# Optimization experiments

Hardware: AMD Instinct MI355X
Metric: run time of the kernel (lower is better)

## Reference

```python
import jax, jax.numpy as jnp
import numpy as np

ALPHA = 2.0
INF = 1e12  # sentinel 'infinity' for the distance transform (fp32-safe)


def _dt1d(f):
    """Exact 1D squared Euclidean distance transform along the last axis.
    d[i] = min_j ( f[j] + (i - j)^2 ).  Brute-force separable form.
    f: [..., N] -> [..., N]
    """
    n = f.shape[-1]
    i = jnp.arange(n, dtype=f.dtype)
    cost = (i[:, None] - i[None, :]) ** 2          # [N, N]
    return jnp.min(f[..., None, :] + cost, axis=-1)


def _edt(mask):
    """Euclidean distance of True pixels to the nearest False pixel
    (matches scipy.ndimage.distance_transform_edt on a binary mask).
    mask: bool [..., H, W] -> float [..., H, W]
    """
    f = jnp.where(mask, jnp.asarray(INF, jnp.float32), 0.0)
    f = _dt1d(f)                                     # pass along W
    f = _dt1d(jnp.swapaxes(f, -1, -2))               # pass along H
    f = jnp.swapaxes(f, -1, -2)
    return jnp.sqrt(jnp.minimum(f, INF))


def _distance_field(imgs):
    """imgs: [B, C, H, W] in [0,1]. Per (b,c): fg_dist/max + bg_dist/max."""
    fg_mask = imgs > 0.5
    bg_mask = ~fg_mask
    fg = _edt(fg_mask)
    bg = _edt(bg_mask)
    fg_any = jnp.any(fg_mask, axis=(-2, -1), keepdims=True)
    bg_any = jnp.any(bg_mask, axis=(-2, -1), keepdims=True)
    fg_n = fg / jnp.maximum(jnp.max(fg, axis=(-2, -1), keepdims=True), 1e-12)
    bg_n = bg / jnp.maximum(jnp.max(bg, axis=(-2, -1), keepdims=True), 1e-12)
    field = jnp.where(fg_any, fg_n + jnp.where(bg_any, bg_n, 0.0), 0.0)
    return field


def setup_inputs() -> dict:
    key = jax.random.key(0)
    k1, k2, k3 = jax.random.split(key, 3)
    B, C, H, W = 4, 2, 256, 256
    preds = jax.random.normal(k1, (B, C, H, W), dtype=jnp.float32)
    targets = jax.random.uniform(k2, (B, C, H, W), dtype=jnp.float32)
    labels = jax.random.randint(k3, (B,), 0, 2).astype(jnp.int64)
    return {"preds": preds, "targets": targets, "labels": labels}


def reference(preds, targets, labels):
    p = jax.nn.sigmoid(preds)
    # distance field is computed under no_grad in the original
    preds_dt = _distance_field(p)
    targets_dt = _distance_field(targets)
    distance = jax.lax.stop_gradient(preds_dt ** ALPHA + targets_dt ** ALPHA)
    preds_error = (p - targets) ** 2
    hd_loss = jnp.mean(preds_error * distance)
    return hd_loss
```

## Files before the change

kernel.cpp:

```cpp
#include <hip/hip_runtime.h>
#include <math.h>

#define HH 256
#define WW 256
#define NIMG 8
#define NF 32
#define FLDSZ (HH * WW)
#define NELEM (NIMG * FLDSZ)
#define LARGE (1 << 27)
#define BIGD (1 << 20)
#define BIGC (1 << 26)

#define BMP_OFF 0
#define BMT_OFF (64u * 1024)
#define APA_OFF (128u * 1024)
#define MPA_OFF (132u * 1024)

__global__ __launch_bounds__(256) void k_bitmap(
    const float* __restrict__ preds, const float* __restrict__ targets,
    unsigned long long* __restrict__ bmP, unsigned long long* __restrict__ bmT)
{
    const int img = blockIdx.x >> 5;
    const int rg  = blockIdx.x & 31;
    const int c   = threadIdx.x;
    const int lane = c & 63, wv = c >> 6;

    const size_t ibase = ((size_t)img * HH + rg * 8) * WW;
#pragma unroll
    for (int r8 = 0; r8 < 8; ++r8) {
        float pv = preds[ibase + r8 * WW + c];
        float tv = targets[ibase + r8 * WW + c];
        unsigned long long bp = __ballot(pv > 0.0f);
        unsigned long long bt = __ballot(tv > 0.5f);
        if (lane == 0) {
            const int row = rg * 8 + r8;
            bmP[((size_t)img * HH + row) * 4 + wv] = bp;
            bmT[((size_t)img * HH + row) * 4 + wv] = bt;
        }
    }
}

__device__ __forceinline__ int win_rowd2(const unsigned long long* __restrict__ sbm,
                                         int j, int wq, int sh)
{
    unsigned long long cur = sbm[j * 4 + wq];
    unsigned long long lw  = (wq > 0) ? sbm[j * 4 + wq - 1] : 0ull;
    unsigned long long rw  = (wq < 3) ? sbm[j * 4 + wq + 1] : 0ull;
    unsigned long long A = cur >> sh;
    if (sh) A |= rw << (64 - sh);
    int dR = A ? __builtin_ctzll(A) : 1000;
    unsigned long long L = (sh == 63) ? cur : (cur & ((1ull << (sh + 1)) - 1ull));
    int dL;
    if (L)       dL = sh - (63 - __builtin_clzll(L));
    else if (lw) dL = sh + 1 + __builtin_clzll(lw);
    else         dL = 1000;
    int d = min(dR, dL);
    return (d <= 255) ? d * d : BIGC;
}

__device__ __forceinline__ int full_rowd(const unsigned long long* __restrict__ sbm,
                                         int j, int c)
{
    int bestd = BIGD;
#pragma unroll
    for (int w = 0; w < 4; ++w) {
        unsigned long long mm = sbm[j * 4 + w];
        if (!mm) continue;
        const int base = w * 64;
        int d;
        if (base + 63 < c) {
            d = c - (base + 63 - __builtin_clzll(mm));
        } else if (base > c) {
            d = base + __builtin_ctzll(mm) - c;
        } else {
            const int t = c - base;
            unsigned long long lowm = (t == 63) ? mm : (mm & ((1ull << (t + 1)) - 1ull));
            unsigned long long him  = mm >> t;
            int dl = lowm ? (t - (63 - __builtin_clzll(lowm))) : BIGD;
            int dr = him  ? __builtin_ctzll(him) : BIGD;
            d = min(dl, dr);
        }
        bestd = min(bestd, d);
    }
    return bestd;
}

__global__ __launch_bounds__(256) void k_dtloss(
    const float* __restrict__ preds, const float* __restrict__ targets,
    const unsigned long long* __restrict__ bmP,
    const unsigned long long* __restrict__ bmT,
    double* __restrict__ Apart, int* __restrict__ Mpart)
{
    const int f   = blockIdx.x >> 4;
    const int rg  = blockIdx.x & 15;
    const int img = f >> 2;
    const int k   = f & 3;
    const int c   = threadIdx.x;
    const int wq  = c >> 6, sh = c & 63;

    __shared__ unsigned long long sbm[HH * 4];

    const unsigned long long* g = (k < 2) ? (bmP + (size_t)img * HH * 4)
                                          : (bmT + (size_t)img * HH * 4);
    const bool inv = ((k & 1) == 0);
#pragma unroll
    for (int q = 0; q < 4; ++q) {
        unsigned long long w = g[q * 256 + c];
        sbm[q * 256 + c] = inv ? ~w : w;
    }
    __syncthreads();

    const int i0 = rg * 16;
    int rw9[9];
#pragma unroll
    for (int q = 0; q < 9; ++q) {
        const int j = i0 - 4 + q;
        rw9[q] = ((unsigned)j < HH) ? win_rowd2(sbm, j, wq, sh) : BIGC;
    }

    double accA = 0.0;
    int mx = 0;

    for (int ii = 0; ii < 16; ++ii) {
        const int i = i0 + ii;

        int best = rw9[4];
        best = min(best, min(rw9[3], rw9[5]) + 1);
        best = min(best, min(rw9[2], rw9[6]) + 4);
        best = min(best, min(rw9[1], rw9[7]) + 9);
        best = min(best, min(rw9[0], rw9[8]) + 16);

        if (__any(best > 16)) {
            int d0 = full_rowd(sbm, i, c);
            int eb = (d0 <= 255) ? d0 * d0 : LARGE;
            for (int r = 1; r < HH; ++r) {
                if (__all(r * r >= eb)) break;
                const int jd = i - r, ju = i + r;
                if (jd >= 0) {
                    int d = full_rowd(sbm, jd, c);
                    if (d <= 255) eb = min(eb, d * d + r * r);
                }
                if (ju < HH) {
                    int d = full_rowd(sbm, ju, c);
                    if (d <= 255) eb = min(eb, d * d + r * r);
                }
            }
            best = eb;
        }

        const size_t idx = ((size_t)img * HH + i) * WW + c;
        float x = preds[idx];
        float t = targets[idx];
        float p = 1.0f / (1.0f + expf(-x));
        float err = (p - t) * (p - t);
        accA += (double)err * (double)best;
        mx = max(mx, best);

#pragma unroll
        for (int q = 0; q < 8; ++q) rw9[q] = rw9[q + 1];
        const int jn = i + 5;
        rw9[8] = ((unsigned)jn < HH) ? win_rowd2(sbm, jn, wq, sh) : BIGC;
    }

#pragma unroll
    for (int off = 32; off > 0; off >>= 1) {
        accA += __shfl_down(accA, off);
        mx = max(mx, __shfl_down(mx, off));
    }
    __shared__ double wA[4];
    __shared__ int    wM[4];
    const int lane = threadIdx.x & 63, wid = threadIdx.x >> 6;
    if (lane == 0) { wA[wid] = accA; wM[wid] = mx; }
    __syncthreads();
    if (threadIdx.x == 0) {
        double a = wA[0] + wA[1] + wA[2] + wA[3];
        int m = max(max(wM[0], wM[1]), max(wM[2], wM[3]));
        Apart[blockIdx.x] = a;
        Mpart[blockIdx.x] = m;
    }
}

__global__ __launch_bounds__(512) void k_final2(
    const double* __restrict__ Apart, const int* __restrict__ Mpart,
    float* __restrict__ out)
{
    const int t = threadIdx.x;
    double v = Apart[t];
    int m = Mpart[t];
#pragma unroll
    for (int off = 8; off > 0; off >>= 1) {
        v += __shfl_down(v, off);
        m = max(m, __shfl_down(m, off));
    }
    __shared__ double sA[NF];
    __shared__ int    sM[NF];
    if ((t & 15) == 0) { sA[t >> 4] = v; sM[t >> 4] = m; }
    __syncthreads();
    if (t == 0) {
        double loss = 0.0;
        for (int img = 0; img < NIMG; ++img) {
            const double a0 = sA[img * 4 + 0], a1 = sA[img * 4 + 1];
            const double a2 = sA[img * 4 + 2], a3 = sA[img * 4 + 3];
            const int m0 = sM[img * 4 + 0], m1 = sM[img * 4 + 1];
            const int m2 = sM[img * 4 + 2], m3 = sM[img * 4 + 3];
            if (m0 > 0) { loss += a0 / (double)m0; if (m1 > 0) loss += a1 / (double)m1; }
            if (m2 > 0) { loss += a2 / (double)m2; if (m3 > 0) loss += a3 / (double)m3; }
        }
        out[0] = (float)(loss / (double)NELEM);
    }
}

extern "C" void kernel_launch(void* const* d_in, const int* in_sizes, int n_in,
                              void* d_out, int out_size, void* d_ws, size_t ws_size,
                              hipStream_t stream)
{
    const float* preds   = (const float*)d_in[0];
    const float* targets = (const float*)d_in[1];
    float* out = (float*)d_out;

    char* ws = (char*)d_ws;
    unsigned long long* bmP = (unsigned long long*)(ws + BMP_OFF);
    unsigned long long* bmT = (unsigned long long*)(ws + BMT_OFF);
    double* Apart           = (double*)(ws + APA_OFF);
    int*    Mpart           = (int*)(ws + MPA_OFF);

    k_bitmap<<<NIMG * 32, 256, 0, stream>>>(preds, targets, bmP, bmT);
    k_dtloss<<<NF * 16,   256, 0, stream>>>(preds, targets, bmP, bmT, Apart, Mpart);
    k_final2<<<1,         512, 0, stream>>>(Apart, Mpart, out);
}
```

Before: 75.09 us.

## Compute all four distance fields per block with shared bitmaps and finer row split

```diff
diff --git a/kernel.cpp b/kernel.cpp
--- a/kernel.cpp
+++ b/kernel.cpp
@@ -14,11 +14,13 @@
 #define BMP_OFF 0
 #define BMT_OFF (64u * 1024)
 #define APA_OFF (128u * 1024)
-#define MPA_OFF (132u * 1024)
+#define MPA_OFF (144u * 1024)
+
+typedef unsigned long long u64;
 
 __global__ __launch_bounds__(256) void k_bitmap(
     const float* __restrict__ preds, const float* __restrict__ targets,
-    unsigned long long* __restrict__ bmP, unsigned long long* __restrict__ bmT)
+    u64* __restrict__ bmP, u64* __restrict__ bmT)
 {
     const int img = blockIdx.x >> 5;
     const int rg  = blockIdx.x & 31;
@@ -30,8 +32,8 @@
     for (int r8 = 0; r8 < 8; ++r8) {
         float pv = preds[ibase + r8 * WW + c];
         float tv = targets[ibase + r8 * WW + c];
-        unsigned long long bp = __ballot(pv > 0.0f);
-        unsigned long long bt = __ballot(tv > 0.5f);
+        u64 bp = __ballot(pv > 0.0f);
+        u64 bt = __ballot(tv > 0.5f);
         if (lane == 0) {
             const int row = rg * 8 + r8;
             bmP[((size_t)img * HH + row) * 4 + wv] = bp;
@@ -40,31 +42,38 @@
     }
 }
 
-__device__ __forceinline__ int win_rowd2(const unsigned long long* __restrict__ sbm,
-                                         int j, int wq, int sh)
-{
-    unsigned long long cur = sbm[j * 4 + wq];
-    unsigned long long lw  = (wq > 0) ? sbm[j * 4 + wq - 1] : 0ull;
-    unsigned long long rw  = (wq < 3) ? sbm[j * 4 + wq + 1] : 0ull;
-    unsigned long long A = cur >> sh;
-    if (sh) A |= rw << (64 - sh);
-    int dR = A ? __builtin_ctzll(A) : 1000;
-    unsigned long long L = (sh == 63) ? cur : (cur & ((1ull << (sh + 1)) - 1ull));
-    int dL;
-    if (L)       dL = sh - (63 - __builtin_clzll(L));
-    else if (lw) dL = sh + 1 + __builtin_clzll(lw);
-    else         dL = 1000;
-    int d = min(dR, dL);
-    return (d <= 255) ? d * d : BIGC;
-}
-
-__device__ __forceinline__ int full_rowd(const unsigned long long* __restrict__ sbm,
-                                         int j, int c)
+__device__ __forceinline__ void win_pair(const u64* __restrict__ sm, int j,
+                                         int wq, int sh, int out[2])
+{
+    const u64 cur = sm[j * 4 + wq];
+    const u64 lwr = (wq > 0) ? sm[j * 4 + wq - 1] : 0ull;
+    const u64 rwr = (wq < 3) ? sm[j * 4 + wq + 1] : 0ull;
+#pragma unroll
+    for (int pol = 0; pol < 2; ++pol) {
+        const u64 cc = pol ? ~cur : cur;
+        const u64 lw = pol ? ((wq > 0) ? ~lwr : 0ull) : lwr;
+        const u64 rw = pol ? ((wq < 3) ? ~rwr : 0ull) : rwr;
+        u64 A = cc >> sh;
+        if (sh) A |= rw << (64 - sh);
+        int dR = A ? __builtin_ctzll(A) : 1000;
+        u64 L = (sh == 63) ? cc : (cc & ((1ull << (sh + 1)) - 1ull));
+        int dL;
+        if (L)       dL = sh - (63 - __builtin_clzll(L));
+        else if (lw) dL = sh + 1 + __builtin_clzll(lw);
+        else         dL = 1000;
+        int d = min(dR, dL);
+        out[pol] = (d <= 255) ? d * d : BIGC;
+    }
+}
+
+__device__ __forceinline__ int full_rowd_f(const u64* __restrict__ sm, int j,
+                                           int c, bool inv)
 {
     int bestd = BIGD;
 #pragma unroll
     for (int w = 0; w < 4; ++w) {
-        unsigned long long mm = sbm[j * 4 + w];
+        u64 mm = sm[j * 4 + w];
+        if (inv) mm = ~mm;
         if (!mm) continue;
         const int base = w * 64;
         int d;
@@ -74,8 +83,8 @@
             d = base + __builtin_ctzll(mm) - c;
         } else {
             const int t = c - base;
-            unsigned long long lowm = (t == 63) ? mm : (mm & ((1ull << (t + 1)) - 1ull));
-            unsigned long long him  = mm >> t;
+            u64 lowm = (t == 63) ? mm : (mm & ((1ull << (t + 1)) - 1ull));
+            u64 him  = mm >> t;
             int dl = lowm ? (t - (63 - __builtin_clzll(lowm))) : BIGD;
             int dr = him  ? __builtin_ctzll(him) : BIGD;
             d = min(dl, dr);
@@ -85,126 +94,174 @@
     return bestd;
 }
 
+__device__ __forceinline__ int exact_scan(const u64* __restrict__ sm, int i,
+                                          int c, bool inv)
+{
+    int d0 = full_rowd_f(sm, i, c, inv);
+    int eb = (d0 <= 255) ? d0 * d0 : LARGE;
+    for (int r = 1; r < HH; ++r) {
+        if (__all(r * r >= eb)) break;
+        const int jd = i - r, ju = i + r;
+        if (jd >= 0) {
+            int d = full_rowd_f(sm, jd, c, inv);
+            if (d <= 255) eb = min(eb, d * d + r * r);
+        }
+        if (ju < HH) {
+            int d = full_rowd_f(sm, ju, c, inv);
+            if (d <= 255) eb = min(eb, d * d + r * r);
+        }
+    }
+    return eb;
+}
+
 __global__ __launch_bounds__(256) void k_dtloss(
     const float* __restrict__ preds, const float* __restrict__ targets,
-    const unsigned long long* __restrict__ bmP,
-    const unsigned long long* __restrict__ bmT,
+    const u64* __restrict__ bmP, const u64* __restrict__ bmT,
     double* __restrict__ Apart, int* __restrict__ Mpart)
 {
-    const int f   = blockIdx.x >> 4;
-    const int rg  = blockIdx.x & 15;
-    const int img = f >> 2;
-    const int k   = f & 3;
+    const int img = blockIdx.x >> 6;
+    const int rg  = blockIdx.x & 63;
     const int c   = threadIdx.x;
     const int wq  = c >> 6, sh = c & 63;
 
-    __shared__ unsigned long long sbm[HH * 4];
-
-    const unsigned long long* g = (k < 2) ? (bmP + (size_t)img * HH * 4)
-                                          : (bmT + (size_t)img * HH * 4);
-    const bool inv = ((k & 1) == 0);
+    __shared__ u64 sp[HH * 4];
+    __shared__ u64 st[HH * 4];
+
 #pragma unroll
     for (int q = 0; q < 4; ++q) {
-        unsigned long long w = g[q * 256 + c];
-        sbm[q * 256 + c] = inv ? ~w : w;
+        sp[q * 256 + c] = bmP[(size_t)img * HH * 4 + q * 256 + c];
+        st[q * 256 + c] = bmT[(size_t)img * HH * 4 + q * 256 + c];
     }
     __syncthreads();
 
-    const int i0 = rg * 16;
-    int rw9[9];
+    const int i0 = rg * 4;
+
+    float xs[4], ts[4];
+#pragma unroll
+    for (int ii = 0; ii < 4; ++ii) {
+        const size_t idx = ((size_t)img * HH + i0 + ii) * WW + c;
+        xs[ii] = preds[idx];
+        ts[ii] = targets[idx];
+    }
+
+    int wPf[9], wPb[9], wTf[9], wTb[9];
 #pragma unroll
     for (int q = 0; q < 9; ++q) {
         const int j = i0 - 4 + q;
-        rw9[q] = ((unsigned)j < HH) ? win_rowd2(sbm, j, wq, sh) : BIGC;
-    }
-
-    double accA = 0.0;
-    int mx = 0;
-
-    for (int ii = 0; ii < 16; ++ii) {
+        if ((unsigned)j < HH) {
+            int prP[2], prT[2];
+            win_pair(sp, j, wq, sh, prP);
+            win_pair(st, j, wq, sh, prT);
+            wPb[q] = prP[0]; wPf[q] = prP[1];
+            wTb[q] = prT[0]; wTf[q] = prT[1];
+        } else {
+            wPb[q] = BIGC; wPf[q] = BIGC; wTb[q] = BIGC; wTf[q] = BIGC;
+        }
+    }
+
+    double a0 = 0.0, a1 = 0.0, a2 = 0.0, a3 = 0.0;
+    int m0 = 0, m1 = 0, m2 = 0, m3 = 0;
+
+#pragma unroll
+    for (int ii = 0; ii < 4; ++ii) {
         const int i = i0 + ii;
 
-        int best = rw9[4];
-        best = min(best, min(rw9[3], rw9[5]) + 1);
-        best = min(best, min(rw9[2], rw9[6]) + 4);
-        best = min(best, min(rw9[1], rw9[7]) + 9);
-        best = min(best, min(rw9[0], rw9[8]) + 16);
-
-        if (__any(best > 16)) {
-            int d0 = full_rowd(sbm, i, c);
-            int eb = (d0 <= 255) ? d0 * d0 : LARGE;
-            for (int r = 1; r < HH; ++r) {
-                if (__all(r * r >= eb)) break;
-                const int jd = i - r, ju = i + r;
-                if (jd >= 0) {
-                    int d = full_rowd(sbm, jd, c);
-                    if (d <= 255) eb = min(eb, d * d + r * r);
-                }
-                if (ju < HH) {
-                    int d = full_rowd(sbm, ju, c);
-                    if (d <= 255) eb = min(eb, d * d + r * r);
-                }
-            }
-            best = eb;
-        }
-
-        const size_t idx = ((size_t)img * HH + i) * WW + c;
-        float x = preds[idx];
-        float t = targets[idx];
-        float p = 1.0f / (1.0f + expf(-x));
-        float err = (p - t) * (p - t);
-        accA += (double)err * (double)best;
-        mx = max(mx, best);
-
-#pragma unroll
-        for (int q = 0; q < 8; ++q) rw9[q] = rw9[q + 1];
+#define COMBINE(w) ({                                             \
+        int _b = w[4];                                            \
+        _b = min(_b, min(w[3], w[5]) + 1);                        \
+        _b = min(_b, min(w[2], w[6]) + 4);                        \
+        _b = min(_b, min(w[1], w[7]) + 9);                        \
+        _b = min(_b, min(w[0], w[8]) + 16); _b; })
+
+        int b0 = COMBINE(wPf);
+        int b1 = COMBINE(wPb);
+        int b2 = COMBINE(wTf);
+        int b3 = COMBINE(wTb);
+
+        if (__any(max(max(b0, b1), max(b2, b3)) > 16)) {
+            if (__any(b0 > 16)) b0 = exact_scan(sp, i, c, true);
+            if (__any(b1 > 16)) b1 = exact_scan(sp, i, c, false);
+            if (__any(b2 > 16)) b2 = exact_scan(st, i, c, true);
+            if (__any(b3 > 16)) b3 = exact_scan(st, i, c, false);
+        }
+
+        float p   = 1.0f / (1.0f + expf(-xs[ii]));
+        float err = (p - ts[ii]) * (p - ts[ii]);
+        const double de = (double)err;
+        a0 += de * (double)b0;  a1 += de * (double)b1;
+        a2 += de * (double)b2;  a3 += de * (double)b3;
+        m0 = max(m0, b0); m1 = max(m1, b1); m2 = max(m2, b2); m3 = max(m3, b3);
+
+#pragma unroll
+        for (int q = 0; q < 8; ++q) {
+            wPf[q] = wPf[q + 1]; wPb[q] = wPb[q + 1];
+            wTf[q] = wTf[q + 1]; wTb[q] = wTb[q + 1];
+        }
         const int jn = i + 5;
-        rw9[8] = ((unsigned)jn < HH) ? win_rowd2(sbm, jn, wq, sh) : BIGC;
+        if ((unsigned)jn < HH) {
+            int prP[2], prT[2];
+            win_pair(sp, jn, wq, sh, prP);
+            win_pair(st, jn, wq, sh, prT);
+            wPb[8] = prP[0]; wPf[8] = prP[1];
+            wTb[8] = prT[0]; wTf[8] = prT[1];
+        } else {
+            wPb[8] = BIGC; wPf[8] = BIGC; wTb[8] = BIGC; wTf[8] = BIGC;
+        }
     }
 
 #pragma unroll
     for (int off = 32; off > 0; off >>= 1) {
-        accA += __shfl_down(accA, off);
-        mx = max(mx, __shfl_down(mx, off));
-    }
-    __shared__ double wA[4];
-    __shared__ int    wM[4];
+        a0 += __shfl_down(a0, off); a1 += __shfl_down(a1, off);
+        a2 += __shfl_down(a2, off); a3 += __shfl_down(a3, off);
+        m0 = max(m0, __shfl_down(m0, off)); m1 = max(m1, __shfl_down(m1, off));
+        m2 = max(m2, __shfl_down(m2, off)); m3 = max(m3, __shfl_down(m3, off));
+    }
+    __shared__ double wA[4][4];
+    __shared__ int    wM[4][4];
     const int lane = threadIdx.x & 63, wid = threadIdx.x >> 6;
-    if (lane == 0) { wA[wid] = accA; wM[wid] = mx; }
+    if (lane == 0) {
+        wA[wid][0] = a0; wA[wid][1] = a1; wA[wid][2] = a2; wA[wid][3] = a3;
+        wM[wid][0] = m0; wM[wid][1] = m1; wM[wid][2] = m2; wM[wid][3] = m3;
+    }
+    __syncthreads();
+    if (threadIdx.x < 4) {
+        const int k = threadIdx.x;
+        double a = wA[0][k] + wA[1][k] + wA[2][k] + wA[3][k];
+        int m = max(max(wM[0][k], wM[1][k]), max(wM[2][k], wM[3][k]));
+        Apart[(size_t)(img * 4 + k) * 64 + rg] = a;
+        Mpart[(size_t)(img * 4 + k) * 64 + rg] = m;
+    }
+}
+
+__global__ __launch_bounds__(1024) void k_final3(
+    const double* __restrict__ Apart, const int* __restrict__ Mpart,
+    float* __restrict__ out)
+{
+    const int lane = threadIdx.x & 63, wave = threadIdx.x >> 6;
+    __shared__ double sA[NF];
+    __shared__ int    sM[NF];
+#pragma unroll
+    for (int rep = 0; rep < 2; ++rep) {
+        const int f = wave * 2 + rep;
+        double v = Apart[f * 64 + lane];
+        int m = Mpart[f * 64 + lane];
+#pragma unroll
+        for (int off = 32; off > 0; off >>= 1) {
+            v += __shfl_down(v, off);
+            m = max(m, __shfl_down(m, off));
+        }
+        if (lane == 0) { sA[f] = v; sM[f] = m; }
+    }
     __syncthreads();
     if (threadIdx.x == 0) {
-        double a = wA[0] + wA[1] + wA[2] + wA[3];
-        int m = max(max(wM[0], wM[1]), max(wM[2], wM[3]));
-        Apart[blockIdx.x] = a;
-        Mpart[blockIdx.x] = m;
-    }
-}
-
-__global__ __launch_bounds__(512) void k_final2(
-    const double* __restrict__ Apart, const int* __restrict__ Mpart,
-    float* __restrict__ out)
-{
-    const int t = threadIdx.x;
-    double v = Apart[t];
-    int m = Mpart[t];
-#pragma unroll
-    for (int off = 8; off > 0; off >>= 1) {
-        v += __shfl_down(v, off);
-        m = max(m, __shfl_down(m, off));
-    }
-    __shared__ double sA[NF];
-    __shared__ int    sM[NF];
-    if ((t & 15) == 0) { sA[t >> 4] = v; sM[t >> 4] = m; }
-    __syncthreads();
-    if (t == 0) {
         double loss = 0.0;
         for (int img = 0; img < NIMG; ++img) {
-            const double a0 = sA[img * 4 + 0], a1 = sA[img * 4 + 1];
-            const double a2 = sA[img * 4 + 2], a3 = sA[img * 4 + 3];
-            const int m0 = sM[img * 4 + 0], m1 = sM[img * 4 + 1];
-            const int m2 = sM[img * 4 + 2], m3 = sM[img * 4 + 3];
-            if (m0 > 0) { loss += a0 / (double)m0; if (m1 > 0) loss += a1 / (double)m1; }
-            if (m2 > 0) { loss += a2 / (double)m2; if (m3 > 0) loss += a3 / (double)m3; }
+            const double A0 = sA[img * 4 + 0], A1 = sA[img * 4 + 1];
+            const double A2 = sA[img * 4 + 2], A3 = sA[img * 4 + 3];
+            const int M0 = sM[img * 4 + 0], M1 = sM[img * 4 + 1];
+            const int M2 = sM[img * 4 + 2], M3 = sM[img * 4 + 3];
+            if (M0 > 0) { loss += A0 / (double)M0; if (M1 > 0) loss += A1 / (double)M1; }
+            if (M2 > 0) { loss += A2 / (double)M2; if (M3 > 0) loss += A3 / (double)M3; }
         }
         out[0] = (float)(loss / (double)NELEM);
     }
@@ -219,12 +276,12 @@
     float* out = (float*)d_out;
 
     char* ws = (char*)d_ws;
-    unsigned long long* bmP = (unsigned long long*)(ws + BMP_OFF);
-    unsigned long long* bmT = (unsigned long long*)(ws + BMT_OFF);
-    double* Apart           = (double*)(ws + APA_OFF);
-    int*    Mpart           = (int*)(ws + MPA_OFF);
+    u64* bmP      = (u64*)(ws + BMP_OFF);
+    u64* bmT      = (u64*)(ws + BMT_OFF);
+    double* Apart = (double*)(ws + APA_OFF);
+    int*    Mpart = (int*)(ws + MPA_OFF);
 
     k_bitmap<<<NIMG * 32, 256, 0, stream>>>(preds, targets, bmP, bmT);
-    k_dtloss<<<NF * 16,   256, 0, stream>>>(preds, targets, bmP, bmT, Apart, Mpart);
-    k_final2<<<1,         512, 0, stream>>>(Apart, Mpart, out);
-}
+    k_dtloss<<<NIMG * 64, 256, 0, stream>>>(preds, targets, bmP, bmT, Apart, Mpart);
+    k_final3<<<1, 1024, 0, stream>>>(Apart, Mpart, out);
+}
```

New measurement: 77.91 us. 3.8% more time.
